# Performance work log

Hardware: AMD Instinct MI355X
Metric: run time of the kernel (lower is better)

## Reference

```python
import jax, jax.numpy as jnp
import numpy as np

N = 100000      # num nodes
E = 800000      # num edges (avg degree 8)
D_IN = 128
D_OUT = 128
ALPHA = 0.5


def setup_inputs() -> dict:
    key = jax.random.key(0)
    ks = jax.random.split(key, 8)
    x = jax.random.normal(ks[0], (N, D_IN), dtype=jnp.float32)
    edge_index = jax.random.randint(ks[1], (2, E), 0, N, dtype=jnp.int64)
    s = 1.0 / np.sqrt(D_IN)
    # lin_self (nn.Linear), and per-direction SAGEConv lin_l (root_weight=False, bias=True)
    W_self = jax.random.uniform(ks[2], (D_IN, D_OUT), jnp.float32, -s, s)
    b_self = jax.random.uniform(ks[3], (D_OUT,), jnp.float32, -s, s)
    W_s2d = jax.random.uniform(ks[4], (D_IN, D_OUT), jnp.float32, -s, s)
    b_s2d = jnp.zeros((D_OUT,), jnp.float32)
    W_d2s = jax.random.uniform(ks[5], (D_IN, D_OUT), jnp.float32, -s, s)
    b_d2s = jnp.zeros((D_OUT,), jnp.float32)
    return {"x": x, "W_self": W_self, "b_self": b_self,
            "W_s2d": W_s2d, "b_s2d": b_s2d,
            "W_d2s": W_d2s, "b_d2s": b_d2s,
            "edge_index": edge_index}


def _mean_aggr(x, gather_idx, scatter_idx, num_nodes):
    # mean of x[gather_idx] segmented by scatter_idx; isolated nodes -> 0 (PyG scatter-mean semantics)
    summed = jax.ops.segment_sum(x[gather_idx], scatter_idx, num_segments=num_nodes)
    cnt = jax.ops.segment_sum(jnp.ones(gather_idx.shape, x.dtype), scatter_idx, num_segments=num_nodes)
    return summed / jnp.maximum(cnt, 1.0)[:, None]


def reference(x, W_self, b_self, W_s2d, b_s2d, W_d2s, b_d2s, edge_index):
    src, dst = edge_index[0], edge_index[1]
    n = x.shape[0]
    # flow='source_to_target': aggregate src features at dst (in-neighbors)
    agg_in = _mean_aggr(x, src, dst, n)
    # flow='target_to_source': aggregate dst features at src (out-neighbors)
    agg_out = _mean_aggr(x, dst, src, n)
    out = (x @ W_self + b_self
           + (1.0 - ALPHA) * (agg_in @ W_s2d + b_s2d)
           + ALPHA * (agg_out @ W_d2s + b_d2s))
    return out
```

## Files before the change

### kernel.cpp

```cpp
#include <hip/hip_runtime.h>


#define D 128
#define KTOT 384
#define NP 16
#define NPSH 4
#define RNGP 12500
#define NCH 48
#define TN 512
#define BT 512

typedef unsigned short u16;
typedef unsigned char u8;
typedef short bf16x8 __attribute__((ext_vector_type(8)));
typedef float f32x4 __attribute__((ext_vector_type(4)));
typedef float f32x2 __attribute__((ext_vector_type(2)));
typedef int i32x4 __attribute__((ext_vector_type(4)));

__device__ __forceinline__ u16 f2bf(float f) {
    unsigned u = __float_as_uint(f);
    unsigned r = (u + 0x7FFF + ((u >> 16) & 1)) >> 16;
    return (u16)r;
}

__device__ __forceinline__ f32x2 shflx2(f32x2 v, int mask) {
    f32x2 r;
    r.x = __shfl_xor(v.x, mask, 32);
    r.y = __shfl_xor(v.y, mask, 32);
    return r;
}

__global__ __launch_bounds__(256) void prep_w_k(const float* __restrict__ W0,
                                                const float* __restrict__ W1,
                                                const float* __restrict__ W2,
                                                const float* __restrict__ b0,
                                                const float* __restrict__ b1,
                                                const float* __restrict__ b2,
                                                u16* __restrict__ Wt,
                                                float* __restrict__ biasc) {
    int idx = blockIdx.x * 256 + threadIdx.x;
    if (idx < 128 * KTOT) {
        int n = idx / KTOT;
        int kt = idx - n * KTOT;
        int seg = kt >> 7;
        int k = kt & 127;
        const float* W = (seg == 0) ? W0 : (seg == 1) ? W1 : W2;
        Wt[n * KTOT + kt] = f2bf(W[k * D + n]);
    }
    if (idx < D) {
        biasc[idx] = b0[idx] + 0.5f * (b1[idx] + b2[idx]);
    }
}

__global__ __launch_bounds__(256) void conv_x_k(const float* __restrict__ x,
                                                u16* __restrict__ Ab,
                                                unsigned* __restrict__ xq,
                                                int N) {
    int gid = blockIdx.x * 256 + threadIdx.x;
    int node = gid >> 5;
    int c = gid & 31;
    if (node >= N) return;
    float4 v = *(const float4*)&x[(size_t)node * D + c * 4];
    ushort4 o;
    o.x = f2bf(v.x); o.y = f2bf(v.y); o.z = f2bf(v.z); o.w = f2bf(v.w);
    *(ushort4*)&Ab[(size_t)node * KTOT + c * 4] = o;
    int q = __builtin_amdgcn_cvt_pk_fp8_f32(v.x, v.y, 0, false);
    q = __builtin_amdgcn_cvt_pk_fp8_f32(v.z, v.w, q, true);
    xq[(size_t)node * 32 + c] = (unsigned)q;
}

__global__ __launch_bounds__(BT) void count_part_k(const int* __restrict__ ei,
                                                   int E, int N, int n2, int S2,
                                                   u8* __restrict__ deg2) {
    __shared__ unsigned cnt[RNGP / 4];
    const int p = blockIdx.x & (NP - 1);
    const int c = blockIdx.x >> NPSH;
    const int lo = p * RNGP;
    const int hi = min(n2, lo + RNGP);
    for (int i = threadIdx.x; i < RNGP / 4; i += BT) cnt[i] = 0;
    __syncthreads();

    const int pc = (((E + NCH - 1) / NCH) + 3) & ~3;
    const int beg = c * pc;
    const int end = min(E, beg + pc);
    for (int e = beg + ((int)threadIdx.x << 2); e < end; e += BT * 4) {
        if (e + 3 < end) {
            i32x4 s4 = __builtin_nontemporal_load((const i32x4*)&ei[e]);
            i32x4 d4 = __builtin_nontemporal_load((const i32x4*)&ei[E + e]);
#pragma unroll
            for (int j = 0; j < 4; ++j) {
                int d = d4[j];
                if (d >= lo && d < hi) {
                    int i = d - lo;
                    atomicAdd(&cnt[i >> 2], 1u << (8 * (i & 3)));
                }
                int os = N + s4[j];
                if (os >= lo && os < hi) {
                    int i = os - lo;
                    atomicAdd(&cnt[i >> 2], 1u << (8 * (i & 3)));
                }
            }
        } else {
            for (int j = 0; j < end - e; ++j) {
                int s = ei[e + j], d = ei[E + e + j];
                if (d >= lo && d < hi) {
                    int i = d - lo;
                    atomicAdd(&cnt[i >> 2], 1u << (8 * (i & 3)));
                }
                int os = N + s;
                if (os >= lo && os < hi) {
                    int i = os - lo;
                    atomicAdd(&cnt[i >> 2], 1u << (8 * (i & 3)));
                }
            }
        }
    }
    __syncthreads();
    unsigned* dst = (unsigned*)(deg2 + (size_t)c * S2 + lo);
    const int spanw = (hi - lo) >> 2;
    for (int i = threadIdx.x; i < spanw; i += BT) dst[i] = cnt[i];
}

__global__ __launch_bounds__(256) void rowscan_k(u8* __restrict__ deg2,
                                                 int* __restrict__ deg,
                                                 int n2, int S2) {
    __shared__ u8 t[NCH][TN];
    const int base = blockIdx.x * TN;
#pragma unroll
    for (int c = 0; c < NCH; ++c) {
        unsigned* src = (unsigned*)&deg2[(size_t)c * S2 + base];
        unsigned* dl = (unsigned*)&t[c][0];
        for (int i = threadIdx.x; i < TN / 4; i += 256) dl[i] = src[i];
    }
    __syncthreads();
    for (int j = threadIdx.x; j < TN; j += 256) {
        int run = 0;
#pragma unroll
        for (int c = 0; c < NCH; ++c) {
            int v = t[c][j];
            t[c][j] = (u8)run;
            run += v;
        }
        if (base + j < n2) deg[base + j] = run;
    }
    __syncthreads();
#pragma unroll
    for (int c = 0; c < NCH; ++c) {
        unsigned* dstg = (unsigned*)&deg2[(size_t)c * S2 + base];
        unsigned* sl = (unsigned*)&t[c][0];
        for (int i = threadIdx.x; i < TN / 4; i += 256) dstg[i] = sl[i];
    }
}

__device__ __forceinline__ int block_incl_scan(int v, int* wsum) {
    int lane = threadIdx.x & 63;
    int wv = threadIdx.x >> 6;
#pragma unroll
    for (int off = 1; off < 64; off <<= 1) {
        int t = __shfl_up(v, off, 64);
        if (lane >= off) v += t;
    }
    if (lane == 63) wsum[wv] = v;
    __syncthreads();
    int add = 0;
    for (int w = 0; w < wv; ++w) add += wsum[w];
    return v + add;
}

__global__ __launch_bounds__(256) void scan1_k(const int* __restrict__ in, int n,
                                               int* __restrict__ bsum) {
    __shared__ int wsum[4];
    int i = blockIdx.x * 256 + threadIdx.x;
    int v = (i < n) ? in[i] : 0;
    int s = block_incl_scan(v, wsum);
    if (threadIdx.x == 255) bsum[blockIdx.x] = s;
}

__global__ __launch_bounds__(1024) void scan2_k(int* __restrict__ bsum, int nb) {
    __shared__ int wsum[16];
    int i = threadIdx.x;
    int v = (i < nb) ? bsum[i] : 0;
    int s = block_incl_scan(v, wsum);
    if (i < nb) bsum[i] = s - v;
}

__global__ __launch_bounds__(256) void scan3_k(const int* __restrict__ in, int n,
                                               const int* __restrict__ bsum,
                                               int* __restrict__ ptr) {
    __shared__ int wsum[4];
    int i = blockIdx.x * 256 + threadIdx.x;
    int v = (i < n) ? in[i] : 0;
    int s = block_incl_scan(v, wsum);
    int off = bsum[blockIdx.x];
    if (i < n) ptr[i] = off + s - v;
    if (i == n - 1) ptr[n] = off + s;
}

__global__ __launch_bounds__(BT) void fill2_part_k(const int* __restrict__ ei,
                                                   int E, int N, int n2, int S2,
                                                   const int* __restrict__ ptr,
                                                   const u8* __restrict__ deg2,
                                                   int* __restrict__ adj) {
    __shared__ unsigned cnt[RNGP / 4];
    const int p = blockIdx.x & (NP - 1);
    const int c = blockIdx.x >> NPSH;
    const int lo = p * RNGP;
    const int hi = min(n2, lo + RNGP);
    const unsigned* d2w = (const unsigned*)(deg2 + (size_t)c * S2 + lo);
    for (int i = threadIdx.x; i < RNGP / 4; i += BT) cnt[i] = d2w[i];
    __syncthreads();

    const int pc = (((E + NCH - 1) / NCH) + 3) & ~3;
    const int beg = c * pc;
    const int end = min(E, beg + pc);
    for (int e = beg + ((int)threadIdx.x << 2); e < end; e += BT * 4) {
        if (e + 3 < end) {
            i32x4 s4 = __builtin_nontemporal_load((const i32x4*)&ei[e]);
            i32x4 d4 = __builtin_nontemporal_load((const i32x4*)&ei[E + e]);
#pragma unroll
            for (int j = 0; j < 4; ++j) {
                int s = s4[j], d = d4[j];
                if (d >= lo && d < hi) {
                    int i = d - lo;
                    unsigned old = atomicAdd(&cnt[i >> 2], 1u << (8 * (i & 3)));
                    int off = (int)((old >> (8 * (i & 3))) & 0xFFu);
                    adj[ptr[d] + off] = s;
                }
                int os = N + s;
                if (os >= lo && os < hi) {
                    int i = os - lo;
                    unsigned old = atomicAdd(&cnt[i >> 2], 1u << (8 * (i & 3)));
                    int off = (int)((old >> (8 * (i & 3))) & 0xFFu);
                    adj[ptr[os] + off] = d;
                }
            }
        } else {
            for (int j = 0; j < end - e; ++j) {
                int s = ei[e + j], d = ei[E + e + j];
                if (d >= lo && d < hi) {
                    int i = d - lo;
                    unsigned old = atomicAdd(&cnt[i >> 2], 1u << (8 * (i & 3)));
                    int off = (int)((old >> (8 * (i & 3))) & 0xFFu);
                    adj[ptr[d] + off] = s;
                }
                int os = N + s;
                if (os >= lo && os < hi) {
                    int i = os - lo;
                    unsigned old = atomicAdd(&cnt[i >> 2], 1u << (8 * (i & 3)));
                    int off = (int)((old >> (8 * (i & 3))) & 0xFFu);
                    adj[ptr[os] + off] = d;
                }
            }
        }
    }
}

__global__ __launch_bounds__(256) void agg_k(const unsigned* __restrict__ xq,
                                             u16* __restrict__ Ab,
                                             const int* __restrict__ ptr,
                                             const int* __restrict__ adj,
                                             int N) {
    int gid = blockIdx.x * 256 + threadIdx.x;
    int node = gid >> 5;
    int lane = gid & 31;
    if (node >= N) return;
    const int dir = blockIdx.y;
    const int ci = dir * N + node;
    const int h2 = lane >> 3;
    const int c16 = lane & 7;

    int beg = ptr[ci], end = ptr[ci + 1];
    f32x2 acc[8];
#pragma unroll
    for (int j = 0; j < 8; ++j) acc[j] = (f32x2){0.f, 0.f};

    for (int j0 = beg; j0 < end; j0 += 32) {
        int a = (j0 + lane < end) ? adj[j0 + lane] : 0;
        int m = min(32, end - j0);
        for (int t = 0; t < m; t += 4) {
            int my = t + h2;
            int nbr = __shfl(a, (my < m) ? my : 0, 32);
            if (my < m) {
                uint4 q = *(const uint4*)((const char*)xq + ((size_t)nbr * 128 + c16 * 16));
                acc[0] += __builtin_amdgcn_cvt_pk_f32_fp8((int)q.x, false);
                acc[1] += __builtin_amdgcn_cvt_pk_f32_fp8((int)q.x, true);
                acc[2] += __builtin_amdgcn_cvt_pk_f32_fp8((int)q.y, false);
                acc[3] += __builtin_amdgcn_cvt_pk_f32_fp8((int)q.y, true);
                acc[4] += __builtin_amdgcn_cvt_pk_f32_fp8((int)q.z, false);
                acc[5] += __builtin_amdgcn_cvt_pk_f32_fp8((int)q.z, true);
                acc[6] += __builtin_amdgcn_cvt_pk_f32_fp8((int)q.w, false);
                acc[7] += __builtin_amdgcn_cvt_pk_f32_fp8((int)q.w, true);
            }
        }
    }
#pragma unroll
    for (int j = 0; j < 8; ++j) {
        acc[j] += shflx2(acc[j], 8);
        acc[j] += shflx2(acc[j], 16);
    }

    if (h2 == 0) {
        float s = 0.5f / fmaxf((float)(end - beg), 1.0f);
        unsigned w[8];
#pragma unroll
        for (int j = 0; j < 8; ++j) {
            w[j] = (unsigned)f2bf(acc[j].x * s) | ((unsigned)f2bf(acc[j].y * s) << 16);
        }
        u16* dst = &Ab[(size_t)node * KTOT + 128 + dir * 128 + c16 * 16];
        *(uint4*)dst = make_uint4(w[0], w[1], w[2], w[3]);
        *(uint4*)(dst + 8) = make_uint4(w[4], w[5], w[6], w[7]);
    }
}

#define BK 64
__global__ __launch_bounds__(256) void gemm_k(const u16* __restrict__ Ab,
                                              const u16* __restrict__ Wt,
                                              const float* __restrict__ biasc,
                                              float* __restrict__ out, int N) {
    __shared__ u16 As[64 * 72];
    __shared__ u16 Bs[128 * 72];

    const int tid = threadIdx.x;
    const int row0 = blockIdx.x * 64;
    const int w = tid >> 6;
    const int lane = tid & 63;
    const int m = lane & 15;
    const int quad = lane >> 4;

    f32x4 acc[8];
#pragma unroll
    for (int t = 0; t < 8; ++t) acc[t] = (f32x4){0.f, 0.f, 0.f, 0.f};

    for (int kb = 0; kb < KTOT / BK; ++kb) {
        const int k0 = kb * BK;
        __syncthreads();
#pragma unroll
        for (int i = 0; i < 2; ++i) {
            int f = tid + i * 256;
            int r = f >> 3;
            int q8 = f & 7;
            int grow = row0 + r;
            uint4 v = make_uint4(0u, 0u, 0u, 0u);
            if (grow < N)
                v = *(const uint4*)&Ab[(size_t)grow * KTOT + k0 + q8 * 8];
            *(uint4*)&As[r * 72 + q8 * 8] = v;
        }
#pragma unroll
        for (int i = 0; i < 4; ++i) {
            int f = tid + i * 256;
            int n = f >> 3;
            int q8 = f & 7;
            uint4 v = *(const uint4*)&Wt[(size_t)n * KTOT + k0 + q8 * 8];
            *(uint4*)&Bs[n * 72 + q8 * 8] = v;
        }
        __syncthreads();

        bf16x8 a[2];
#pragma unroll
        for (int s = 0; s < 2; ++s)
            a[s] = *(const bf16x8*)&As[(w * 16 + m) * 72 + s * 32 + quad * 8];
#pragma unroll
        for (int t = 0; t < 8; ++t) {
#pragma unroll
            for (int s = 0; s < 2; ++s) {
                bf16x8 b = *(const bf16x8*)&Bs[(t * 16 + m) * 72 + s * 32 + quad * 8];
                acc[t] = __builtin_amdgcn_mfma_f32_16x16x32_bf16(a[s], b, acc[t], 0, 0, 0);
            }
        }
    }

    const int rowbase = row0 + w * 16 + quad * 4;
#pragma unroll
    for (int t = 0; t < 8; ++t) {
        int col = t * 16 + m;
        float b = biasc[col];
#pragma unroll
        for (int r = 0; r < 4; ++r) {
            int row = rowbase + r;
            if (row < N) out[(size_t)row * D + col] = acc[t][r] + b;
        }
    }
}


extern "C" void kernel_launch(void* const* d_in, const int* in_sizes, int n_in,
                              void* d_out, int out_size, void* d_ws, size_t ws_size,
                              hipStream_t stream) {
    const float* x      = (const float*)d_in[0];
    const float* W_self = (const float*)d_in[1];
    const float* b_self = (const float*)d_in[2];
    const float* W_s2d  = (const float*)d_in[3];
    const float* b_s2d  = (const float*)d_in[4];
    const float* W_d2s  = (const float*)d_in[5];
    const float* b_d2s  = (const float*)d_in[6];
    const int*   ei     = (const int*)d_in[7];

    const int N = in_sizes[0] / D;
    const int E = in_sizes[7] / 2;
    float* out = (float*)d_out;
    char* ws = (char*)d_ws;

    const int n2 = 2 * N;
    const int S2 = ((n2 + TN - 1) / TN) * TN;

    size_t o = 0;
    u16* Ab = (u16*)(ws + o);        o += (size_t)N * KTOT * sizeof(u16);
    unsigned* xq = (unsigned*)(ws + o); o += (size_t)N * 32 * sizeof(unsigned);
    u16* Wt = (u16*)(ws + o);        o += (size_t)D * KTOT * sizeof(u16);
    float* biasc = (float*)(ws + o); o += D * sizeof(float);
    int* deg = (int*)(ws + o);       o += (size_t)n2 * sizeof(int);
    int* ptr = (int*)(ws + o);       o += ((size_t)n2 + 1) * sizeof(int);
    u8* deg2 = (u8*)(ws + o);        o += (size_t)NCH * S2 * sizeof(u8);
    int* adj = (int*)(ws + o);       o += (size_t)2 * E * sizeof(int);
    int* bs  = (int*)(ws + o);       o += 1024 * sizeof(int);

    const int nb2 = (n2 + 255) / 256;
    const int node32_blocks = (int)(((size_t)N * 32 + 255) / 256);
    const int gemm_blocks = (N + 63) / 64;
    const int cs_grid = NCH * NP;
    const int rs_grid = S2 / TN;

    prep_w_k<<<(128 * KTOT + 255) / 256, 256, 0, stream>>>(W_self, W_s2d, W_d2s,
                                                           b_self, b_s2d, b_d2s,
                                                           Wt, biasc);
    conv_x_k<<<node32_blocks, 256, 0, stream>>>(x, Ab, xq, N);

    count_part_k<<<cs_grid, BT, 0, stream>>>(ei, E, N, n2, S2, deg2);
    rowscan_k<<<rs_grid, 256, 0, stream>>>(deg2, deg, n2, S2);
    scan1_k<<<nb2, 256, 0, stream>>>(deg, n2, bs);
    scan2_k<<<1, 1024, 0, stream>>>(bs, nb2);
    scan3_k<<<nb2, 256, 0, stream>>>(deg, n2, bs, ptr);
    fill2_part_k<<<cs_grid, BT, 0, stream>>>(ei, E, N, n2, S2, ptr, deg2, adj);

    dim3 agrid(node32_blocks, 2);
    agg_k<<<agrid, 256, 0, stream>>>(xq, Ab, ptr, adj, N);

    gemm_k<<<gemm_blocks, 256, 0, stream>>>(Ab, Wt, biasc, out, N);
}
```

Baseline: 272.3 us.

## Aggregate each node with 8 lanes instead of 32 and drop cross-lane reduction

The mean-aggregation kernel now assigns 8 lanes per node, with each lane owning 16 fp8 features and looping over all neighbors serially, instead of 32 lanes splitting neighbors four ways. This removes the xor-shuffle reduction and the idle lanes at write-out, and quarters the number of threads launched. Rounding to bf16 now uses a hardware packed conversion instruction. The trade-off is less memory-level parallelism per node and longer serial loops for high-degree nodes, which could hurt latency hiding.

```diff
diff --git a/kernel.cpp b/kernel.cpp
--- a/kernel.cpp
+++ b/kernel.cpp
@@ -23,10 +23,9 @@
     return (u16)r;
 }
 
-__device__ __forceinline__ f32x2 shflx2(f32x2 v, int mask) {
-    f32x2 r;
-    r.x = __shfl_xor(v.x, mask, 32);
-    r.y = __shfl_xor(v.y, mask, 32);
+__device__ __forceinline__ unsigned cvt_pk_bf16(float a, float b) {
+    unsigned r;
+    asm("v_cvt_pk_bf16_f32 %0, %1, %2" : "=v"(r) : "v"(a), "v"(b));
     return r;
 }
 
@@ -261,55 +260,42 @@
                                              const int* __restrict__ adj,
                                              int N) {
     int gid = blockIdx.x * 256 + threadIdx.x;
-    int node = gid >> 5;
-    int lane = gid & 31;
+    int node = gid >> 3;
+    int l8 = gid & 7;
     if (node >= N) return;
     const int dir = blockIdx.y;
     const int ci = dir * N + node;
-    const int h2 = lane >> 3;
-    const int c16 = lane & 7;
 
     int beg = ptr[ci], end = ptr[ci + 1];
     f32x2 acc[8];
 #pragma unroll
     for (int j = 0; j < 8; ++j) acc[j] = (f32x2){0.f, 0.f};
 
-    for (int j0 = beg; j0 < end; j0 += 32) {
-        int a = (j0 + lane < end) ? adj[j0 + lane] : 0;
-        int m = min(32, end - j0);
-        for (int t = 0; t < m; t += 4) {
-            int my = t + h2;
-            int nbr = __shfl(a, (my < m) ? my : 0, 32);
-            if (my < m) {
-                uint4 q = *(const uint4*)((const char*)xq + ((size_t)nbr * 128 + c16 * 16));
-                acc[0] += __builtin_amdgcn_cvt_pk_f32_fp8((int)q.x, false);
-                acc[1] += __builtin_amdgcn_cvt_pk_f32_fp8((int)q.x, true);
-                acc[2] += __builtin_amdgcn_cvt_pk_f32_fp8((int)q.y, false);
-                acc[3] += __builtin_amdgcn_cvt_pk_f32_fp8((int)q.y, true);
-                acc[4] += __builtin_amdgcn_cvt_pk_f32_fp8((int)q.z, false);
-                acc[5] += __builtin_amdgcn_cvt_pk_f32_fp8((int)q.z, true);
-                acc[6] += __builtin_amdgcn_cvt_pk_f32_fp8((int)q.w, false);
-                acc[7] += __builtin_amdgcn_cvt_pk_f32_fp8((int)q.w, true);
-            }
-        }
-    }
-#pragma unroll
-    for (int j = 0; j < 8; ++j) {
-        acc[j] += shflx2(acc[j], 8);
-        acc[j] += shflx2(acc[j], 16);
-    }
-
-    if (h2 == 0) {
-        float s = 0.5f / fmaxf((float)(end - beg), 1.0f);
-        unsigned w[8];
-#pragma unroll
-        for (int j = 0; j < 8; ++j) {
-            w[j] = (unsigned)f2bf(acc[j].x * s) | ((unsigned)f2bf(acc[j].y * s) << 16);
-        }
-        u16* dst = &Ab[(size_t)node * KTOT + 128 + dir * 128 + c16 * 16];
-        *(uint4*)dst = make_uint4(w[0], w[1], w[2], w[3]);
-        *(uint4*)(dst + 8) = make_uint4(w[4], w[5], w[6], w[7]);
-    }
+    for (int j0 = beg; j0 < end; j0 += 8) {
+        int a = (j0 + l8 < end) ? adj[j0 + l8] : 0;
+        int m = min(8, end - j0);
+        for (int t = 0; t < m; ++t) {
+            int nbr = __shfl(a, t, 8);
+            uint4 q = *(const uint4*)((const char*)xq + ((size_t)nbr * 128 + l8 * 16));
+            acc[0] += __builtin_amdgcn_cvt_pk_f32_fp8((int)q.x, false);
+            acc[1] += __builtin_amdgcn_cvt_pk_f32_fp8((int)q.x, true);
+            acc[2] += __builtin_amdgcn_cvt_pk_f32_fp8((int)q.y, false);
+            acc[3] += __builtin_amdgcn_cvt_pk_f32_fp8((int)q.y, true);
+            acc[4] += __builtin_amdgcn_cvt_pk_f32_fp8((int)q.z, false);
+            acc[5] += __builtin_amdgcn_cvt_pk_f32_fp8((int)q.z, true);
+            acc[6] += __builtin_amdgcn_cvt_pk_f32_fp8((int)q.w, false);
+            acc[7] += __builtin_amdgcn_cvt_pk_f32_fp8((int)q.w, true);
+        }
+    }
+
+    float s = 0.5f / fmaxf((float)(end - beg), 1.0f);
+    unsigned w[8];
+#pragma unroll
+    for (int j = 0; j < 8; ++j)
+        w[j] = cvt_pk_bf16(acc[j].x * s, acc[j].y * s);
+    u16* dst = &Ab[(size_t)node * KTOT + 128 + dir * 128 + l8 * 16];
+    *(uint4*)dst = make_uint4(w[0], w[1], w[2], w[3]);
+    *(uint4*)(dst + 8) = make_uint4(w[4], w[5], w[6], w[7]);
 }
 
 #define BK 64
@@ -416,6 +402,7 @@
 
     const int nb2 = (n2 + 255) / 256;
     const int node32_blocks = (int)(((size_t)N * 32 + 255) / 256);
+    const int node8_blocks = (int)(((size_t)N * 8 + 255) / 256);
     const int gemm_blocks = (N + 63) / 64;
     const int cs_grid = NCH * NP;
     const int rs_grid = S2 / TN;
@@ -432,7 +419,7 @@
     scan3_k<<<nb2, 256, 0, stream>>>(deg, n2, bs, ptr);
     fill2_part_k<<<cs_grid, BT, 0, stream>>>(ei, E, N, n2, S2, ptr, deg2, adj);
 
-    dim3 agrid(node32_blocks, 2);
+    dim3 agrid(node8_blocks, 2);
     agg_k<<<agrid, 256, 0, stream>>>(xq, Ab, ptr, adj, N);
 
     gemm_k<<<gemm_blocks, 256, 0, stream>>>(Ab, Wt, biasc, out, N);
```

Result: faster. 262.5 us (-3.6%).
